# Optimization experiments

Measured on AMD Instinct MI355X. Metric: run time of the kernel, lower is better.

The kernel has to match this reference:

```python
import jax, jax.numpy as jnp
from jax import lax
import numpy as np

KERNEL_SIZE = 29
N_T = 1000
SIGMA_MIN, SIGMA_MAX = 0.5, 20.0
HIDDEN = 32


def _gaussian_kernel1d(sigma, ksize):
    # torchvision: linspace over [-half, half], normalized gaussian pdf
    half = (ksize - 1) * 0.5
    xg = jnp.linspace(-half, half, ksize)
    pdf = jnp.exp(-0.5 * (xg / sigma) ** 2)
    return pdf / pdf.sum()


def batch_blur(x, sigmas, ksize=KERNEL_SIZE):
    # x: [B,C,H,W], sigmas: [B]. Per-sample separable gaussian blur as a single
    # grouped depthwise conv (feature_group_count = B*C) instead of a Python loop.
    B, C, H, W = x.shape
    k1 = jax.vmap(lambda s: _gaussian_kernel1d(s, ksize))(sigmas)  # [B, k]
    pad = ksize // 2
    xp = jnp.pad(x, ((0, 0), (0, 0), (pad, pad), (pad, pad)), mode='reflect')
    lhs = xp.reshape(1, B * C, H + 2 * pad, W + 2 * pad)
    kbc = jnp.repeat(k1, C, axis=0)  # [B*C, k] per-channel kernel
    # vertical pass then horizontal pass (outer-product 2D kernel == two 1D passes)
    y = lax.conv_general_dilated(lhs, kbc[:, None, :, None], (1, 1), 'VALID',
                                 feature_group_count=B * C)
    y = lax.conv_general_dilated(y, kbc[:, None, None, :], (1, 1), 'VALID',
                                 feature_group_count=B * C)
    return y.reshape(B, C, H, W)


def gt_net(z, tn, W1, b1, tw, W2, b2):
    # simple time-conditioned conv net standing in for the opaque `gt` module
    h = lax.conv_general_dilated(z, W1, (1, 1), 'SAME')  # [B,HIDDEN,H,W]
    h = h + b1[None, :, None, None] + (tn[:, None] * tw[None, :])[:, :, None, None]
    h = jax.nn.relu(h)
    out = lax.conv_general_dilated(h, W2, (1, 1), 'SAME') + b2[None, :, None, None]
    return out


def setup_inputs() -> dict:
    key = jax.random.key(0)
    ks = jax.random.split(key, 6)
    B, C, H, W = 32, 3, 256, 256
    x = jax.random.normal(ks[0], (B, C, H, W), dtype=jnp.float32)
    t = jax.random.randint(ks[1], (B,), 0, N_T, dtype=jnp.int32)
    W1 = jax.random.normal(ks[2], (HIDDEN, C, 3, 3), dtype=jnp.float32) * 0.1
    b1 = jnp.zeros((HIDDEN,), dtype=jnp.float32)
    tw = jax.random.normal(ks[3], (HIDDEN,), dtype=jnp.float32) * 0.1
    W2 = jax.random.normal(ks[4], (C, HIDDEN, 3, 3), dtype=jnp.float32) * 0.1
    b2 = jnp.zeros((C,), dtype=jnp.float32)
    sigma_schedule = jnp.linspace(SIGMA_MIN, SIGMA_MAX, N_T, dtype=jnp.float32)
    return {"x": x, "t": t, "W1": W1, "b1": b1, "tw": tw, "W2": W2, "b2": b2,
            "sigma_schedule": sigma_schedule}


def reference(x, t, W1, b1, tw, W2, b2, sigma_schedule):
    sigma_t = sigma_schedule[t]                      # [B]
    z_t = batch_blur(x, sigma_t, KERNEL_SIZE)        # [B,C,H,W]
    preds = gt_net(z_t, t.astype(jnp.float32) / N_T, W1, b1, tw, W2, b2)
    return jnp.mean((x - preds) ** 2)                # MSELoss
```

## Files before the change

kernel.cpp:

```cpp
#include <hip/hip_runtime.h>
#include <hip/hip_bf16.h>

#define BATCH 32
#define CH 3
#define HH 256
#define WW 256
#define KS 29
#define PAD 14
#define NT_F 1000.0f

typedef __attribute__((ext_vector_type(8))) short short8;
typedef __attribute__((ext_vector_type(4))) float f32x4;

union U4 { short8 s8; uint4 u4; };

__device__ inline unsigned short bf16rne(float f) {
  unsigned u = __float_as_uint(f);
  unsigned r = (u + 0x7FFFu + ((u >> 16) & 1u)) >> 16;
  return (unsigned short)r;
}
__device__ inline unsigned pk_bf16(float a, float b) {
  union { __hip_bfloat162 h2; unsigned u; } cv;
  cv.h2 = __float22bfloat162_rn(make_float2(a, b));
  return cv.u;
}


#define PARTIAL_OFF 3150656

__global__ __launch_bounds__(256, 3) void blur_kernel(
    const float* __restrict__ x, const int* __restrict__ t,
    const float* __restrict__ sched, const float* __restrict__ W1,
    const float* __restrict__ b1, const float* __restrict__ tw,
    const float* __restrict__ W2, float* __restrict__ ws,
    unsigned short* __restrict__ z) {
  int blk = blockIdx.x;
  int tid = threadIdx.x;

  if (blk >= BATCH * CH * 8) {
    float* tcond = ws + 1024;
    unsigned short* w1k = (unsigned short*)(ws + 2048);
    unsigned short* w1g = (unsigned short*)(ws + 2560);
    unsigned short* w2c = (unsigned short*)(ws + 2624);
    for (int i = tid; i < 1024; i += 256) {
      int o = i >> 5, k = i & 31;
      int q = k >> 3, j = k & 7, ci = j & 3;
      int dy, dx;
      if (q < 3) { dy = q; dx = j >> 2; } else { dy = j >> 2; dx = 2; }
      w1k[i] = (ci < 3) ? bf16rne(W1[o * 27 + ci * 9 + dy * 3 + dx]) : (unsigned short)0;
    }
    for (int i = tid; i < 128; i += 256) {
      int o = i >> 2, j = i & 3;
      w1g[i] = (j < 3) ? bf16rne(W1[o * 27 + j * 9 + 8]) : (unsigned short)0;
    }
    for (int i = tid; i < 4608; i += 256) {
      int tap = i >> 9, r = i & 511;
      int n = r >> 5, kn = r & 31;
      int och = (kn >> 1) + ((kn & 1) ? 16 : 0);
      int dy = tap / 3, dx = tap - dy * 3;
      w2c[i] = (n < 3) ? bf16rne(W2[((n * 32 + och) * 3 + dy) * 3 + dx])
                       : (unsigned short)0;
    }
    for (int i = tid; i < 1024; i += 256) {
      int b = i >> 5, o = i & 31;
      tcond[i] = b1[o] + ((float)t[b] * (1.0f / NT_F)) * tw[o];
    }
    return;
  }

  __shared__ float vsp[32][288];
  __shared__ float gkl[32];
  int rg = blk & 7;
  int bc = blk >> 3;
  int b = bc / CH;
  int y0 = rg * 32;
  const float* xp = x + (size_t)bc * (HH * WW);

  float xv[60];
#pragma unroll
  for (int i = 0; i < 60; i++) {
    int gy = y0 - PAD + i;
    gy = (gy < 0) ? -gy : gy;
    gy = (gy >= HH) ? (2 * HH - 2 - gy) : gy;
    xv[i] = xp[gy * WW + tid];
  }

  if (tid < 64) {
    float wexp = 0.0f;
    if (tid < KS) {
      float sigma = sched[t[b]];
      float xg = (float)(tid - PAD) / sigma;
      wexp = expf(-0.5f * xg * xg);
    }
    float s = wexp;
#pragma unroll
    for (int off = 32; off > 0; off >>= 1) s += __shfl_down(s, off);
    float tot = __shfl(s, 0);
    if (tid < 32) gkl[tid] = wexp / tot;
  }
  __syncthreads();

  float acc[32];
#pragma unroll
  for (int yy = 0; yy < 32; yy++) acc[yy] = 0.0f;
#pragma unroll
  for (int kk = 0; kk < KS; kk++) {
    float kv = gkl[kk];
#pragma unroll
    for (int yy = 0; yy < 32; yy++) acc[yy] += kv * xv[yy + kk];
  }
#pragma unroll
  for (int yy = 0; yy < 32; yy++) vsp[yy][tid + 16] = acc[yy];
  __syncthreads();
  {
    int row = tid >> 4, i2 = tid & 15;
#pragma unroll
    for (int r2 = 0; r2 < 2; r2++) {
      int rr = row + 16 * r2;
      vsp[rr][i2] = vsp[rr][32 - i2];
      vsp[rr][272 + i2] = vsp[rr][270 - i2];
    }
  }
  __syncthreads();

  size_t zb = (size_t)bc * (HH * WW);
#pragma unroll
  for (int it = 0; it < 8; ++it) {
    int unit = tid + 256 * it;
    int row = unit >> 6, cg = unit & 63;
    float w[36];
#pragma unroll
    for (int i = 0; i < 9; i++)
      *(float4*)&w[4 * i] = *(const float4*)&vsp[row][4 * (cg + i)];
    float o0 = 0, o1 = 0, o2 = 0, o3 = 0;
#pragma unroll
    for (int kk = 0; kk < KS; kk++) {
      float kv = gkl[kk];
      o0 += kv * w[2 + kk];
      o1 += kv * w[3 + kk];
      o2 += kv * w[4 + kk];
      o3 += kv * w[5 + kk];
    }
    unsigned u0 = pk_bf16(o0, o1);
    unsigned u1 = pk_bf16(o2, o3);
    *(uint2*)&z[zb + (size_t)(y0 + row) * WW + 4 * cg] = make_uint2(u0, u1);
  }
}

__global__ __launch_bounds__(256, 5) void convloss_kernel(
    const float* __restrict__ x, const float* __restrict__ ws,
    const float* __restrict__ b2g, float* __restrict__ partial) {
  __shared__ __align__(16) unsigned short zs4[400 * 4];
  __shared__ __align__(16) unsigned short hs[324 * 40];
  __shared__ float wsum[4];

  const float* tcond = ws + 1024;
  const unsigned short* w1k = (const unsigned short*)(ws + 2048);
  const unsigned short* w1g = (const unsigned short*)(ws + 2560);
  const unsigned short* w2c = (const unsigned short*)(ws + 2624);
  const unsigned short* zg = (const unsigned short*)(ws + 4928);

  int bx = blockIdx.x, by = blockIdx.y, b = blockIdx.z;
  int tid = threadIdx.x;
  int x0 = bx * 16, y0 = by * 16;
  const unsigned short* zbp = zg + (size_t)b * 3 * HH * WW;

  int lane = tid & 63;
  int q = lane >> 4;
  int col = lane & 15;
  int wv = tid >> 6;

#pragma unroll
  for (int r = 0; r < 2; r++) {
    int unit = tid + 256 * r;
    if (unit < 400) {
      int zy = unit / 20, zx = unit - zy * 20;
      int gy = y0 - 2 + zy, gx = x0 - 2 + zx;
      unsigned c0 = 0, c1 = 0, c2 = 0;
      if ((unsigned)gy < (unsigned)HH && (unsigned)gx < (unsigned)WW) {
        int gi = gy * WW + gx;
        c0 = zbp[gi];
        c1 = zbp[HH * WW + gi];
        c2 = zbp[2 * HH * WW + gi];
      }
      *(uint2*)&zs4[unit * 4] = make_uint2(c0 | (c1 << 16), c2);
    }
  }

  const float* xb = x + (size_t)b * 3 * HH * WW;
  int colc = (col < 3) ? col : 0;
  float4 xpre[4];
#pragma unroll
  for (int i = 0; i < 4; i++) {
    int g2 = wv * 4 + i;
    xpre[i] = *(const float4*)&xb[colc * (HH * WW) + (y0 + g2) * WW + x0 + q * 4];
  }

  U4 B1a, B1b, B2a, B2b;
  B1a.u4 = *(const uint4*)(w1k + col * 32 + q * 8);
  B1b.u4 = *(const uint4*)(w1k + (col + 16) * 32 + q * 8);
  {
    uint2 ta = *(const uint2*)(w1g + col * 4);
    uint2 tb = *(const uint2*)(w1g + (col + 16) * 4);
    bool q0 = (q == 0);
    B2a.u4 = make_uint4(q0 ? ta.x : 0u, q0 ? ta.y : 0u, 0u, 0u);
    B2b.u4 = make_uint4(q0 ? tb.x : 0u, q0 ? tb.y : 0u, 0u, 0u);
  }
  float tc0 = tcond[b * 32 + col];
  float tc1 = tcond[b * 32 + 16 + col];
  float b2v = b2g[colc];
  const f32x4 tcv0 = {tc0, tc0, tc0, tc0};
  const f32x4 tcv1 = {tc1, tc1, tc1, tc1};

  __syncthreads();

  int dyq = (q < 3) ? q : 0;
  int dxq = (q < 3) ? 0 : 2;
  int strBpx = (q < 3) ? 1 : 20;

#pragma unroll
  for (int i = 0; i < 6; i++) {
    int g = wv + 4 * i;
    if (g < 21) {
      int py_a, px_a;
      if (g < 18) {
        py_a = g; px_a = col;
      } else {
        int u = (g - 18) * 16 + col;
        u = (u > 35) ? 35 : u;
        py_a = u >> 1; px_a = 16 + (u & 1);
      }
      int lo_i = (py_a + dyq) * 20 + px_a + dxq;
      uint2 lo = *(const uint2*)&zs4[lo_i * 4];
      uint2 hi = *(const uint2*)&zs4[(lo_i + strBpx) * 4];
      U4 A1;
      A1.u4 = make_uint4(lo.x, lo.y, hi.x, hi.y);
      uint2 t2 = *(const uint2*)&zs4[((py_a + 2) * 20 + px_a + 2) * 4];
      U4 A2;
      bool q0 = (q == 0);
      A2.u4 = make_uint4(q0 ? t2.x : 0u, q0 ? t2.y : 0u, 0u, 0u);
      f32x4 acc0 = __builtin_amdgcn_mfma_f32_16x16x32_bf16(A1.s8, B1a.s8, tcv0, 0, 0, 0);
      acc0 = __builtin_amdgcn_mfma_f32_16x16x32_bf16(A2.s8, B2a.s8, acc0, 0, 0, 0);
      f32x4 acc1 = __builtin_amdgcn_mfma_f32_16x16x32_bf16(A1.s8, B1b.s8, tcv1, 0, 0, 0);
      acc1 = __builtin_amdgcn_mfma_f32_16x16x32_bf16(A2.s8, B2b.s8, acc1, 0, 0, 0);
      if (g < 18) {
        int pb = (g * 18 + q * 4) * 40 + 2 * col;
#pragma unroll
        for (int r = 0; r < 4; r++) {
          unsigned pk = pk_bf16(fmaxf(acc0[r], 0.0f), fmaxf(acc1[r], 0.0f));
          *(unsigned*)&hs[pb + r * 40] = pk;
        }
      } else {
        int ub = (g - 18) * 16 + q * 4;
#pragma unroll
        for (int r = 0; r < 4; r++) {
          int u2 = ub + r;
          u2 = (u2 > 35) ? 35 : u2;
          unsigned pk = pk_bf16(fmaxf(acc0[r], 0.0f), fmaxf(acc1[r], 0.0f));
          *(unsigned*)&hs[((u2 >> 1) * 18 + 16 + (u2 & 1)) * 40 + 2 * col] = pk;
        }
      }
    }
  }
  __syncthreads();

  const f32x4 bcv = {b2v, b2v, b2v, b2v};
  f32x4 dacc[4];
#pragma unroll
  for (int i = 0; i < 4; i++) dacc[i] = bcv;
  {
    const unsigned short* hbase = &hs[((wv * 4) * 18 + col) * 40 + q * 8];
#pragma unroll
    for (int dx = 0; dx < 3; dx++) {
      U4 Bt0, Bt1, Bt2;
      Bt0.u4 = *(const uint4*)(w2c + (0 * 3 + dx) * 512 + col * 32 + q * 8);
      Bt1.u4 = *(const uint4*)(w2c + (1 * 3 + dx) * 512 + col * 32 + q * 8);
      Bt2.u4 = *(const uint4*)(w2c + (2 * 3 + dx) * 512 + col * 32 + q * 8);
#pragma unroll
      for (int rr = 0; rr < 6; rr++) {
        U4 A;
        A.u4 = *(const uint4*)&hbase[(rr * 18 + dx) * 40];
        if (rr < 4)
          dacc[rr] = __builtin_amdgcn_mfma_f32_16x16x32_bf16(A.s8, Bt0.s8, dacc[rr], 0, 0, 0);
        if (rr >= 1 && rr < 5)
          dacc[rr - 1] = __builtin_amdgcn_mfma_f32_16x16x32_bf16(A.s8, Bt1.s8, dacc[rr - 1], 0, 0, 0);
        if (rr >= 2)
          dacc[rr - 2] = __builtin_amdgcn_mfma_f32_16x16x32_bf16(A.s8, Bt2.s8, dacc[rr - 2], 0, 0, 0);
      }
    }
  }

  float s = 0.0f;
  if (col < 3) {
#pragma unroll
    for (int i = 0; i < 4; i++) {
      float4 xv = xpre[i];
      float d0 = xv.x - dacc[i][0];
      float d1 = xv.y - dacc[i][1];
      float d2 = xv.z - dacc[i][2];
      float d3 = xv.w - dacc[i][3];
      s += d0 * d0 + d1 * d1 + d2 * d2 + d3 * d3;
    }
  }
#pragma unroll
  for (int off = 32; off > 0; off >>= 1) s += __shfl_down(s, off);
  if (lane == 0) wsum[wv] = s;
  __syncthreads();
  if (tid == 0) {
    int bid = (b * 16 + by) * 16 + bx;
    partial[bid] = wsum[0] + wsum[1] + wsum[2] + wsum[3];
  }
}

__global__ __launch_bounds__(256) void reduce_kernel(const float* __restrict__ partial,
                                                     float* __restrict__ out) {
  __shared__ float wsum[4];
  int tid = threadIdx.x;
  float s = 0.0f;
#pragma unroll
  for (int i = 0; i < 8; i++) {
    float4 v = *(const float4*)&partial[(tid + 256 * i) * 4];
    s += v.x + v.y + v.z + v.w;
  }
#pragma unroll
  for (int off = 32; off > 0; off >>= 1) s += __shfl_down(s, off);
  if ((tid & 63) == 0) wsum[tid >> 6] = s;
  __syncthreads();
  if (tid == 0)
    out[0] = (wsum[0] + wsum[1] + wsum[2] + wsum[3]) * (1.0f / 6291456.0f);
}

extern "C" void kernel_launch(void* const* d_in, const int* in_sizes, int n_in,
                              void* d_out, int out_size, void* d_ws, size_t ws_size,
                              hipStream_t stream) {
  const float* x = (const float*)d_in[0];
  const int* t = (const int*)d_in[1];
  const float* W1 = (const float*)d_in[2];
  const float* b1 = (const float*)d_in[3];
  const float* tw = (const float*)d_in[4];
  const float* W2 = (const float*)d_in[5];
  const float* b2 = (const float*)d_in[6];
  const float* sched = (const float*)d_in[7];
  float* out = (float*)d_out;
  float* ws = (float*)d_ws;
  unsigned short* z = (unsigned short*)(ws + 4928);
  float* partial = ws + PARTIAL_OFF;

  blur_kernel<<<BATCH * CH * 8 + 1, 256, 0, stream>>>(x, t, sched, W1, b1, tw, W2, ws, z);
  dim3 grid(16, 16, BATCH);
  convloss_kernel<<<grid, 256, 0, stream>>>(x, ws, b2, partial);
  reduce_kernel<<<1, 256, 0, stream>>>(partial, out);
}
```

Baseline: 141.5 us.

## Recast first conv as 32x32x16 MFMA with weights as A operand

The first 3x3 conv (3→32 channels) now uses 32x32x16 bf16 MFMAs with the packed weights as the A matrix and 32 pixels per wave as B, instead of pairs of 16x16x32 MFMAs over 16-pixel groups with a special-case tail. The weight layout is rebuilt as three 16-wide K chunks of taps×channels, and the W2 packing no longer interleaves channels, matching the new hidden-activation layout. The x prefetch moves after the first phase. The intent is fewer MFMA issues and simpler LDS indexing; the cost is zero-padded K lanes and a changed workspace layout.

```diff
diff --git a/kernel.cpp b/kernel.cpp
--- a/kernel.cpp
+++ b/kernel.cpp
@@ -11,6 +11,7 @@
 
 typedef __attribute__((ext_vector_type(8))) short short8;
 typedef __attribute__((ext_vector_type(4))) float f32x4;
+typedef __attribute__((ext_vector_type(16))) float f32x16;
 
 union U4 { short8 s8; uint4 u4; };
 
@@ -26,7 +27,7 @@
 }
 
 
-#define PARTIAL_OFF 3150656
+#define PARTIAL_OFF 3151872
 
 __global__ __launch_bounds__(256, 3) void blur_kernel(
     const float* __restrict__ x, const int* __restrict__ t,
@@ -39,24 +40,18 @@
 
   if (blk >= BATCH * CH * 8) {
     float* tcond = ws + 1024;
-    unsigned short* w1k = (unsigned short*)(ws + 2048);
-    unsigned short* w1g = (unsigned short*)(ws + 2560);
-    unsigned short* w2c = (unsigned short*)(ws + 2624);
-    for (int i = tid; i < 1024; i += 256) {
-      int o = i >> 5, k = i & 31;
-      int q = k >> 3, j = k & 7, ci = j & 3;
-      int dy, dx;
-      if (q < 3) { dy = q; dx = j >> 2; } else { dy = j >> 2; dx = 2; }
-      w1k[i] = (ci < 3) ? bf16rne(W1[o * 27 + ci * 9 + dy * 3 + dx]) : (unsigned short)0;
-    }
-    for (int i = tid; i < 128; i += 256) {
-      int o = i >> 2, j = i & 3;
-      w1g[i] = (j < 3) ? bf16rne(W1[o * 27 + j * 9 + 8]) : (unsigned short)0;
+    unsigned short* w1n = (unsigned short*)(ws + 2048);
+    unsigned short* w2c = (unsigned short*)(ws + 2816);
+    for (int i = tid; i < 1536; i += 256) {
+      int mf = i >> 9, r = i & 511;
+      int och = r >> 4, s = r & 15;
+      int tp = mf * 4 + (s >> 2), ci = s & 3;
+      w1n[i] = (ci < 3 && tp < 9) ? bf16rne(W1[och * 27 + ci * 9 + tp])
+                                  : (unsigned short)0;
     }
     for (int i = tid; i < 4608; i += 256) {
       int tap = i >> 9, r = i & 511;
-      int n = r >> 5, kn = r & 31;
-      int och = (kn >> 1) + ((kn & 1) ? 16 : 0);
+      int n = r >> 5, och = r & 31;
       int dy = tap / 3, dx = tap - dy * 3;
       w2c[i] = (n < 3) ? bf16rne(W2[((n * 32 + och) * 3 + dy) * 3 + dx])
                        : (unsigned short)0;
@@ -155,10 +150,9 @@
   __shared__ float wsum[4];
 
   const float* tcond = ws + 1024;
-  const unsigned short* w1k = (const unsigned short*)(ws + 2048);
-  const unsigned short* w1g = (const unsigned short*)(ws + 2560);
-  const unsigned short* w2c = (const unsigned short*)(ws + 2624);
-  const unsigned short* zg = (const unsigned short*)(ws + 4928);
+  const unsigned short* w1n = (const unsigned short*)(ws + 2048);
+  const unsigned short* w2c = (const unsigned short*)(ws + 2816);
+  const unsigned short* zg = (const unsigned short*)(ws + 5120);
 
   int bx = blockIdx.x, by = blockIdx.y, b = blockIdx.z;
   int tid = threadIdx.x;
@@ -168,6 +162,8 @@
   int lane = tid & 63;
   int q = lane >> 4;
   int col = lane & 15;
+  int col32 = lane & 31;
+  int h = lane >> 5;
   int wv = tid >> 6;
 
 #pragma unroll
@@ -187,82 +183,69 @@
     }
   }
 
+  U4 W0, W1f, W2f;
+  W0.u4  = *(const uint4*)(w1n + 0 * 512 + col32 * 16 + h * 8);
+  W1f.u4 = *(const uint4*)(w1n + 1 * 512 + col32 * 16 + h * 8);
+  W2f.u4 = *(const uint4*)(w1n + 2 * 512 + col32 * 16 + h * 8);
+
+  f32x16 tc16;
+#pragma unroll
+  for (int r1 = 0; r1 < 4; r1++) {
+    float4 v = *(const float4*)(tcond + b * 32 + 4 * h + 8 * r1);
+    tc16[4 * r1 + 0] = v.x;
+    tc16[4 * r1 + 1] = v.y;
+    tc16[4 * r1 + 2] = v.z;
+    tc16[4 * r1 + 3] = v.w;
+  }
+
+  int colc = (col < 3) ? col : 0;
+  float b2v = b2g[colc];
+
+  __syncthreads();
+
+  int oA0 = h ? 8 : 0, oB0 = h ? 80 : 4;
+  int oA1 = h ? 160 : 84, oB1 = h ? 164 : 88;
+  const int oA2 = 168;
+
+#pragma unroll
+  for (int i = 0; i < 3; i++) {
+    int g = wv + 4 * i;
+    if (g < 11) {
+      int p = g * 32 + col32;
+      int pc = (p > 323) ? 323 : p;
+      int py = pc / 18, px = pc - py * 18;
+      int ub = (py * 20 + px) * 4;
+      uint2 l0 = *(const uint2*)&zs4[ub + oA0];
+      uint2 l1 = *(const uint2*)&zs4[ub + oB0];
+      uint2 l2 = *(const uint2*)&zs4[ub + oA1];
+      uint2 l3 = *(const uint2*)&zs4[ub + oB1];
+      uint2 l4 = *(const uint2*)&zs4[ub + oA2];
+      U4 Bz0, Bz1, Bz2;
+      Bz0.u4 = make_uint4(l0.x, l0.y, l1.x, l1.y);
+      Bz1.u4 = make_uint4(l2.x, l2.y, l3.x, l3.y);
+      Bz2.u4 = make_uint4(l4.x, l4.y, 0u, 0u);
+      f32x16 a = __builtin_amdgcn_mfma_f32_32x32x16_bf16(W0.s8, Bz0.s8, tc16, 0, 0, 0);
+      a = __builtin_amdgcn_mfma_f32_32x32x16_bf16(W1f.s8, Bz1.s8, a, 0, 0, 0);
+      a = __builtin_amdgcn_mfma_f32_32x32x16_bf16(W2f.s8, Bz2.s8, a, 0, 0, 0);
+      if (p < 324) {
+#pragma unroll
+        for (int r1 = 0; r1 < 4; r1++) {
+          unsigned u0 = pk_bf16(fmaxf(a[4 * r1 + 0], 0.0f), fmaxf(a[4 * r1 + 1], 0.0f));
+          unsigned u1 = pk_bf16(fmaxf(a[4 * r1 + 2], 0.0f), fmaxf(a[4 * r1 + 3], 0.0f));
+          *(uint2*)&hs[p * 40 + 4 * h + 8 * r1] = make_uint2(u0, u1);
+        }
+      }
+    }
+  }
+  __syncthreads();
+
   const float* xb = x + (size_t)b * 3 * HH * WW;
-  int colc = (col < 3) ? col : 0;
   float4 xpre[4];
 #pragma unroll
   for (int i = 0; i < 4; i++) {
     int g2 = wv * 4 + i;
     xpre[i] = *(const float4*)&xb[colc * (HH * WW) + (y0 + g2) * WW + x0 + q * 4];
   }
-
-  U4 B1a, B1b, B2a, B2b;
-  B1a.u4 = *(const uint4*)(w1k + col * 32 + q * 8);
-  B1b.u4 = *(const uint4*)(w1k + (col + 16) * 32 + q * 8);
-  {
-    uint2 ta = *(const uint2*)(w1g + col * 4);
-    uint2 tb = *(const uint2*)(w1g + (col + 16) * 4);
-    bool q0 = (q == 0);
-    B2a.u4 = make_uint4(q0 ? ta.x : 0u, q0 ? ta.y : 0u, 0u, 0u);
-    B2b.u4 = make_uint4(q0 ? tb.x : 0u, q0 ? tb.y : 0u, 0u, 0u);
-  }
-  float tc0 = tcond[b * 32 + col];
-  float tc1 = tcond[b * 32 + 16 + col];
-  float b2v = b2g[colc];
-  const f32x4 tcv0 = {tc0, tc0, tc0, tc0};
-  const f32x4 tcv1 = {tc1, tc1, tc1, tc1};
-
-  __syncthreads();
-
-  int dyq = (q < 3) ? q : 0;
-  int dxq = (q < 3) ? 0 : 2;
-  int strBpx = (q < 3) ? 1 : 20;
-
-#pragma unroll
-  for (int i = 0; i < 6; i++) {
-    int g = wv + 4 * i;
-    if (g < 21) {
-      int py_a, px_a;
-      if (g < 18) {
-        py_a = g; px_a = col;
-      } else {
-        int u = (g - 18) * 16 + col;
-        u = (u > 35) ? 35 : u;
-        py_a = u >> 1; px_a = 16 + (u & 1);
-      }
-      int lo_i = (py_a + dyq) * 20 + px_a + dxq;
-      uint2 lo = *(const uint2*)&zs4[lo_i * 4];
-      uint2 hi = *(const uint2*)&zs4[(lo_i + strBpx) * 4];
-      U4 A1;
-      A1.u4 = make_uint4(lo.x, lo.y, hi.x, hi.y);
-      uint2 t2 = *(const uint2*)&zs4[((py_a + 2) * 20 + px_a + 2) * 4];
-      U4 A2;
-      bool q0 = (q == 0);
-      A2.u4 = make_uint4(q0 ? t2.x : 0u, q0 ? t2.y : 0u, 0u, 0u);
-      f32x4 acc0 = __builtin_amdgcn_mfma_f32_16x16x32_bf16(A1.s8, B1a.s8, tcv0, 0, 0, 0);
-      acc0 = __builtin_amdgcn_mfma_f32_16x16x32_bf16(A2.s8, B2a.s8, acc0, 0, 0, 0);
-      f32x4 acc1 = __builtin_amdgcn_mfma_f32_16x16x32_bf16(A1.s8, B1b.s8, tcv1, 0, 0, 0);
-      acc1 = __builtin_amdgcn_mfma_f32_16x16x32_bf16(A2.s8, B2b.s8, acc1, 0, 0, 0);
-      if (g < 18) {
-        int pb = (g * 18 + q * 4) * 40 + 2 * col;
-#pragma unroll
-        for (int r = 0; r < 4; r++) {
-          unsigned pk = pk_bf16(fmaxf(acc0[r], 0.0f), fmaxf(acc1[r], 0.0f));
-          *(unsigned*)&hs[pb + r * 40] = pk;
-        }
-      } else {
-        int ub = (g - 18) * 16 + q * 4;
-#pragma unroll
-        for (int r = 0; r < 4; r++) {
-          int u2 = ub + r;
-          u2 = (u2 > 35) ? 35 : u2;
-          unsigned pk = pk_bf16(fmaxf(acc0[r], 0.0f), fmaxf(acc1[r], 0.0f));
-          *(unsigned*)&hs[((u2 >> 1) * 18 + 16 + (u2 & 1)) * 40 + 2 * col] = pk;
-        }
-      }
-    }
-  }
-  __syncthreads();
 
   const f32x4 bcv = {b2v, b2v, b2v, b2v};
   f32x4 dacc[4];
@@ -343,7 +326,7 @@
   const float* sched = (const float*)d_in[7];
   float* out = (float*)d_out;
   float* ws = (float*)d_ws;
-  unsigned short* z = (unsigned short*)(ws + 4928);
+  unsigned short* z = (unsigned short*)(ws + 5120);
   float* partial = ws + PARTIAL_OFF;
 
   blur_kernel<<<BATCH * CH * 8 + 1, 256, 0, stream>>>(x, t, sched, W1, b1, tw, W2, ws, z);
```

New measurement: 140.6 us. Within noise of the previous version (-0.7%).
